# Optimization experiments

Measured on AMD Instinct MI355X. Metric: run time of the kernel, lower is better.

## Reference

```python
import jax, jax.numpy as jnp
import numpy as np
from jax import lax

B, T, D = 1, 2048, 2048
H, KVH, HD = 16, 4, 128
BETA = 0.9
ROPE_BASE = 10000.0


def _causal_prefix_ema(x, beta):
    # x: (B, T, D); m_t = beta * m_{t-1} + (1 - beta) * x_t, m_{-1} = 0
    def step(m, xt):
        m = beta * m + (1.0 - beta) * xt
        return m, m
    _, ys = lax.scan(step, jnp.zeros_like(x[:, 0]), jnp.swapaxes(x, 0, 1))
    return jnp.swapaxes(ys, 0, 1)


def _rotate_half(x):
    x1, x2 = jnp.split(x, 2, axis=-1)
    return jnp.concatenate([-x2, x1], axis=-1)


def _rope_cos_sin(t, hd, dtype):
    inv_freq = 1.0 / (ROPE_BASE ** (jnp.arange(0, hd, 2, dtype=jnp.float32) / hd))
    freqs = jnp.arange(t, dtype=jnp.float32)[:, None] * inv_freq[None, :]  # (T, HD/2)
    emb = jnp.concatenate([freqs, freqs], axis=-1)  # (T, HD)
    return jnp.cos(emb).astype(dtype)[None, None], jnp.sin(emb).astype(dtype)[None, None]


def setup_inputs() -> dict:
    key = jax.random.key(0)
    ks = jax.random.split(key, 8)
    std = 0.02
    return {
        "hidden_states": jax.random.normal(ks[0], (B, T, D), jnp.float32),
        "Wq": jax.random.normal(ks[1], (D, H * HD), jnp.float32) * std,
        "Wk": jax.random.normal(ks[2], (D, KVH * HD), jnp.float32) * std,
        "Wv": jax.random.normal(ks[3], (D, KVH * HD), jnp.float32) * std,
        "Wo": jax.random.normal(ks[4], (H * HD, D), jnp.float32) * std,
        "Wr1": jax.random.normal(ks[5], (D, D // 2), jnp.float32) * std,
        "br1": jnp.zeros((D // 2,), jnp.float32),
        "Wr2": jax.random.normal(ks[6], (D // 2, 2), jnp.float32) * std,
        "br2": jnp.zeros((2,), jnp.float32),
    }


def reference(hidden_states, Wq, Wk, Wv, Wo, Wr1, br1, Wr2, br2):
    b, t, d = hidden_states.shape
    q = hidden_states @ Wq  # (B, T, H*HD)

    # multi-level memories: l1 = raw, l2 = causal prefix EMA
    l2 = _causal_prefix_ema(hidden_states, BETA)

    # router MLP on q + softmax over levels
    h = jax.nn.silu(q @ Wr1 + br1)
    lam = jax.nn.softmax(h @ Wr2 + br2, axis=-1)  # (B, T, 2)
    fused = lam[..., 0:1] * hidden_states + lam[..., 1:2] * l2

    # shape to heads
    q_s = q.reshape(b, t, H, HD).transpose(0, 2, 1, 3)                 # (B, H, T, HD)
    k_s = (fused @ Wk).reshape(b, t, KVH, HD).transpose(0, 2, 1, 3)    # (B, KVH, T, HD)
    v_s = (fused @ Wv).reshape(b, t, KVH, HD).transpose(0, 2, 1, 3)

    # RoPE
    cos, sin = _rope_cos_sin(t, HD, q_s.dtype)
    q_s = q_s * cos + _rotate_half(q_s) * sin
    k_s = k_s * cos + _rotate_half(k_s) * sin

    # repeat kv for GQA
    n_rep = H // KVH
    k_s = jnp.repeat(k_s, n_rep, axis=1)
    v_s = jnp.repeat(v_s, n_rep, axis=1)

    # causal SDPA
    scale = 1.0 / jnp.sqrt(jnp.asarray(HD, q_s.dtype))
    scores = jnp.einsum("bhqd,bhkd->bhqk", q_s, k_s) * scale
    causal = jnp.tril(jnp.ones((t, t), dtype=bool))
    scores = jnp.where(causal[None, None], scores, jnp.finfo(scores.dtype).min)
    attn = jax.nn.softmax(scores, axis=-1)
    out = jnp.einsum("bhqk,bhkd->bhqd", attn, v_s)  # (B, H, T, HD)

    out = out.transpose(0, 2, 1, 3).reshape(b, t, H * HD)
    return out @ Wo
```

## Files before the change

### kernel.cpp

```cpp
#include <hip/hip_runtime.h>
#include <hip/hip_bf16.h>

#define T_SEQ 2048
#define D_MODEL 2048
#define NH 16
#define NKVH 4
#define HD 128

typedef __attribute__((ext_vector_type(8))) short bf16x8;
typedef __attribute__((ext_vector_type(4))) float f32x4;

static __device__ __forceinline__ short f32_to_bf16(float f) {
    unsigned u = __float_as_uint(f);
    u += 0x7fffu + ((u >> 16) & 1u);
    return (short)(u >> 16);
}
static __device__ __forceinline__ float bf16_to_f32(short s) {
    return __uint_as_float(((unsigned)(unsigned short)s) << 16);
}
static __device__ __forceinline__ void gl_to_lds16(const void* g, void* l) {
    __builtin_amdgcn_global_load_lds(
        (const __attribute__((address_space(1))) unsigned int*)g,
        (__attribute__((address_space(3))) unsigned int*)l, 16, 0, 0);
}

template<int BN>
__global__ __launch_bounds__(256, 2) void gemm_bt_kernel(
    const short* __restrict__ A, const short* __restrict__ Bt,
    float* __restrict__ Cf, short* __restrict__ Cb,
    int M, int N, int K, const float* __restrict__ bias, int act)
{
    constexpr int NI = BN / 64;
    constexpr int BCH = BN / 32;
    __shared__ short Alds[3][64 * 64];
    __shared__ short Blds[3][BN * 64];

    const int tid = threadIdx.x;
    const int wave = tid >> 6, lane = tid & 63;
    const int l16 = lane & 15, quad = lane >> 4;
    const int wn = wave * (BN / 4);
    const int m0 = blockIdx.y * 64, n0 = blockIdx.x * BN;
    const int niter = K >> 6;

    f32x4 acc[4][NI] = {};

    #pragma unroll
    for (int st = 0; st < 2; ++st) {
        int kk0 = st << 6;
        #pragma unroll
        for (int p = 0; p < 2; ++p) {
            int li = p * 256 + tid;
            int row = li >> 3, sc = li & 7;
            gl_to_lds16(A + (size_t)(m0 + row) * K + kk0 + ((sc ^ (row & 7)) * 8),
                        &Alds[st][(size_t)(p * 256 + wave * 64) * 8]);
        }
        #pragma unroll
        for (int p = 0; p < BCH; ++p) {
            int li = p * 256 + tid;
            int row = li >> 3, sc = li & 7;
            gl_to_lds16(Bt + (size_t)(n0 + row) * K + kk0 + ((sc ^ (row & 7)) * 8),
                        &Blds[st][(size_t)(p * 256 + wave * 64) * 8]);
        }
    }

    int cur = 0, stg = 2;
    for (int t = 0; t < niter; ++t) {
        if (t + 1 < niter) {
            if constexpr (BN == 128)
                asm volatile("s_waitcnt vmcnt(6)\n\ts_barrier" ::: "memory");
            else
                asm volatile("s_waitcnt vmcnt(4)\n\ts_barrier" ::: "memory");
        } else {
            asm volatile("s_waitcnt vmcnt(0)\n\ts_barrier" ::: "memory");
        }

        if (t + 2 < niter) {
            int k1 = (t + 2) << 6;
            #pragma unroll
            for (int p = 0; p < 2; ++p) {
                int li = p * 256 + tid;
                int row = li >> 3, sc = li & 7;
                gl_to_lds16(A + (size_t)(m0 + row) * K + k1 + ((sc ^ (row & 7)) * 8),
                            &Alds[stg][(size_t)(p * 256 + wave * 64) * 8]);
            }
            #pragma unroll
            for (int p = 0; p < BCH; ++p) {
                int li = p * 256 + tid;
                int row = li >> 3, sc = li & 7;
                gl_to_lds16(Bt + (size_t)(n0 + row) * K + k1 + ((sc ^ (row & 7)) * 8),
                            &Blds[stg][(size_t)(p * 256 + wave * 64) * 8]);
            }
        }

        const short* Ab = Alds[cur];
        const short* Bb = Blds[cur];
        #pragma unroll
        for (int kk = 0; kk < 2; ++kk) {
            bf16x8 a[4], b[NI];
            #pragma unroll
            for (int i = 0; i < 4; ++i)
                a[i] = *(const bf16x8*)
                    &Ab[(size_t)(i * 16 + l16) * 64 + (((kk * 4 + quad) ^ (l16 & 7)) * 8)];
            #pragma unroll
            for (int i = 0; i < NI; ++i)
                b[i] = *(const bf16x8*)
                    &Bb[(size_t)(wn + i * 16 + l16) * 64 + (((kk * 4 + quad) ^ (l16 & 7)) * 8)];
            #pragma unroll
            for (int mi = 0; mi < 4; ++mi)
                #pragma unroll
                for (int ni = 0; ni < NI; ++ni)
                    acc[mi][ni] = __builtin_amdgcn_mfma_f32_16x16x32_bf16(
                        a[mi], b[ni], acc[mi][ni], 0, 0, 0);
        }
        cur = (cur == 2) ? 0 : cur + 1;
        stg = (stg == 2) ? 0 : stg + 1;
    }

    #pragma unroll
    for (int mi = 0; mi < 4; ++mi) {
        #pragma unroll
        for (int ni = 0; ni < NI; ++ni) {
            int col = n0 + wn + ni * 16 + l16;
            float bv = bias ? bias[col] : 0.0f;
            #pragma unroll
            for (int r = 0; r < 4; ++r) {
                int row = m0 + mi * 16 + quad * 4 + r;
                float x = acc[mi][ni][r] + bv;
                if (act) x = x / (1.0f + __expf(-x));
                size_t o = (size_t)row * N + col;
                if (Cf) Cf[o] = x;
                if (Cb) Cb[o] = f32_to_bf16(x);
            }
        }
    }
}

__global__ __launch_bounds__(256) void transpose_all_kernel(
    const float* __restrict__ Wq, const float* __restrict__ Wk,
    const float* __restrict__ Wv, const float* __restrict__ Wr1,
    const float* __restrict__ Wo, short* __restrict__ Wq_t,
    short* __restrict__ Wkv_t, short* __restrict__ Wr1_t,
    short* __restrict__ Wo_t)
{
    __shared__ float tile[32][33];
    int bx = blockIdx.x;
    const float* src; short* dst; int ld, cb;
    if (bx < 64)       { src = Wq;  dst = Wq_t;  ld = 2048; cb = bx; }
    else if (bx < 80)  { src = Wk;  dst = Wkv_t; ld = 512;  cb = bx - 64; }
    else if (bx < 96)  { src = Wv;  dst = Wkv_t + (size_t)512 * 2048; ld = 512; cb = bx - 80; }
    else if (bx < 128) { src = Wr1; dst = Wr1_t; ld = 1024; cb = bx - 96; }
    else               { src = Wo;  dst = Wo_t;  ld = 2048; cb = bx - 128; }
    int c0 = cb * 32, r0 = blockIdx.y * 32;
    int t = threadIdx.x;
    int r = t >> 3, c4 = (t & 7) * 4;
    float4 v = *(const float4*)&src[(size_t)(r0 + r) * ld + c0 + c4];
    tile[r][c4 + 0] = v.x; tile[r][c4 + 1] = v.y;
    tile[r][c4 + 2] = v.z; tile[r][c4 + 3] = v.w;
    __syncthreads();
    short o[4];
    #pragma unroll
    for (int j = 0; j < 4; ++j) o[j] = f32_to_bf16(tile[c4 + j][r]);
    *(uint2*)&dst[(size_t)(c0 + r) * 2048 + r0 + c4] = *(const uint2*)o;
}

__global__ __launch_bounds__(256) void transpose_bf_kernel(
    const short* __restrict__ src, int ld, short* __restrict__ dst, int ldd)
{
    __shared__ float tile[32][33];
    int r0 = blockIdx.y * 32, c0 = blockIdx.x * 32;
    int x = threadIdx.x & 31, y = threadIdx.x >> 5;
    #pragma unroll
    for (int i = 0; i < 4; ++i)
        tile[y + i * 8][x] = bf16_to_f32(src[(size_t)(r0 + y + i * 8) * ld + c0 + x]);
    __syncthreads();
    #pragma unroll
    for (int i = 0; i < 4; ++i)
        dst[(size_t)(c0 + y + i * 8) * ldd + r0 + x] = f32_to_bf16(tile[x][y + i * 8]);
}

__global__ __launch_bounds__(256) void ema_kernel(const float* __restrict__ hs,
                                                  float* __restrict__ l2,
                                                  short* __restrict__ hs_b)
{
    int d = blockIdx.y * 256 + threadIdx.x;
    int t0 = blockIdx.x * 128;
    int ts = t0 - 192; if (ts < 0) ts = 0;
    float m = 0.0f;
    for (int tb = ts; tb < t0; tb += 16) {
        float buf[16];
        #pragma unroll
        for (int j = 0; j < 16; ++j) buf[j] = hs[(size_t)(tb + j) * D_MODEL + d];
        #pragma unroll
        for (int j = 0; j < 16; ++j) m = 0.9f * m + 0.1f * buf[j];
    }
    for (int tb = t0; tb < t0 + 128; tb += 16) {
        float buf[16];
        #pragma unroll
        for (int j = 0; j < 16; ++j) buf[j] = hs[(size_t)(tb + j) * D_MODEL + d];
        #pragma unroll
        for (int j = 0; j < 16; ++j) hs_b[(size_t)(tb + j) * D_MODEL + d] = f32_to_bf16(buf[j]);
        #pragma unroll
        for (int j = 0; j < 16; ++j) { m = 0.9f * m + 0.1f * buf[j]; buf[j] = m; }
        #pragma unroll
        for (int j = 0; j < 16; ++j) l2[(size_t)(tb + j) * D_MODEL + d] = buf[j];
    }
}

__global__ __launch_bounds__(64) void lam_kernel(
    const short* __restrict__ h, const float* __restrict__ Wr2,
    const float* __restrict__ br2, float* __restrict__ lam)
{
    int t = blockIdx.x;
    int lane = threadIdx.x;
    float z0 = 0.0f, z1 = 0.0f;
    for (int i = lane; i < 1024; i += 64) {
        float hv = bf16_to_f32(h[(size_t)t * 1024 + i]);
        z0 += hv * Wr2[i * 2 + 0];
        z1 += hv * Wr2[i * 2 + 1];
    }
    #pragma unroll
    for (int off = 1; off < 64; off <<= 1) {
        z0 += __shfl_xor(z0, off);
        z1 += __shfl_xor(z1, off);
    }
    if (lane == 0) {
        z0 += br2[0]; z1 += br2[1];
        float mx = fmaxf(z0, z1);
        float e0 = expf(z0 - mx), e1 = expf(z1 - mx);
        float inv = 1.0f / (e0 + e1);
        lam[t * 2 + 0] = e0 * inv;
        lam[t * 2 + 1] = e1 * inv;
    }
}

__global__ void fuse_kernel(const float* __restrict__ hs, const float* __restrict__ l2,
                            const float* __restrict__ lam, short* __restrict__ fused)
{
    int idx = blockIdx.x * blockDim.x + threadIdx.x;
    int t = idx >> 9;
    float a0 = lam[t * 2 + 0], a1 = lam[t * 2 + 1];
    float4 a = ((const float4*)hs)[idx];
    float4 b = ((const float4*)l2)[idx];
    short o[4] = {f32_to_bf16(a0 * a.x + a1 * b.x), f32_to_bf16(a0 * a.y + a1 * b.y),
                  f32_to_bf16(a0 * a.z + a1 * b.z), f32_to_bf16(a0 * a.w + a1 * b.w)};
    *(uint2*)(fused + (size_t)idx * 4) = *(const uint2*)o;
}

__global__ void rope_q_kernel(const short* __restrict__ q, short* __restrict__ qr)
{
    int idx = blockIdx.x * blockDim.x + threadIdx.x;
    int d = idx & 63;
    int h = (idx >> 6) & 15;
    int t = idx >> 10;
    float fr = (float)t * __expf(-(float)d * 0.14391156831212787f);
    float s, c;
    sincosf(fr, &s, &c);
    const float sc = 0.08838834764831845f;
    const short* src = q + (size_t)t * D_MODEL + h * HD;
    float x1 = bf16_to_f32(src[d]) * sc, x2 = bf16_to_f32(src[d + 64]) * sc;
    short* dst = qr + ((size_t)h * T_SEQ + t) * HD;
    dst[d]      = f32_to_bf16(x1 * c - x2 * s);
    dst[d + 64] = f32_to_bf16(x2 * c + x1 * s);
}

__global__ void rope_k_kernel(const short* __restrict__ kv, short* __restrict__ kr)
{
    int idx = blockIdx.x * blockDim.x + threadIdx.x;
    int d = idx & 63;
    int kh = (idx >> 6) & 3;
    int t = idx >> 8;
    float fr = (float)t * __expf(-(float)d * 0.14391156831212787f);
    float s, c;
    sincosf(fr, &s, &c);
    const short* src = kv + (size_t)t * 1024 + kh * HD;
    float x1 = bf16_to_f32(src[d]), x2 = bf16_to_f32(src[d + 64]);
    short* dst = kr + ((size_t)kh * T_SEQ + t) * HD;
    dst[d]      = f32_to_bf16(x1 * c - x2 * s);
    dst[d + 64] = f32_to_bf16(x2 * c + x1 * s);
}

__global__ __launch_bounds__(512, 2) void attn_kernel(
    const short* __restrict__ Qr, const short* __restrict__ Kr,
    const short* __restrict__ Vt, short* __restrict__ Out)
{
    const int h = blockIdx.x;
    const int y = blockIdx.y;
    const int kvh = h >> 2;
    const int tid = threadIdx.x;
    const int wave = tid >> 6, lane = tid & 63;
    const int l16 = lane & 15, quad = lane >> 4;
    const int wq = wave & 1;
    const int wk = wave >> 1;

    __shared__ __align__(16) char smem[147456];
    short* Klds = (short*)smem;
    short* Vlds = (short*)(smem + 65536);
    short* Plds = (short*)(smem + 131072);

    const short* kbase = Kr + (size_t)kvh * T_SEQ * HD;
    const short* vbase = Vt + (size_t)kvh * HD * T_SEQ;

    #pragma unroll 1
    for (int ph = 0; ph < 2; ++ph) {
        const int qt32 = ph ? (31 - y) : y;
        const int qbase = qt32 * 64 + wq * 32;
        const int n = (qt32 >> 1) + 1;
        const int ko = wk * 32;

        bf16x8 qf[2][4];
        #pragma unroll
        for (int m = 0; m < 2; ++m) {
            const short* qrow = Qr + ((size_t)h * T_SEQ + qbase + m * 16 + l16) * HD;
            #pragma unroll
            for (int kc = 0; kc < 4; ++kc)
                qf[m][kc] = *(const bf16x8*)&qrow[kc * 32 + quad * 8];
        }
        f32x4 o[2][8] = {};
        float lsum[2][4] = {};

        __syncthreads();

        {
            #pragma unroll
            for (int p = 0; p < 4; ++p) {
                int li = p * 512 + tid;
                int row = li >> 4, gs = (li & 15) ^ (row & 15);
                gl_to_lds16(kbase + (size_t)row * HD + gs * 8,
                            &Klds[(size_t)(p * 512 + wave * 64) * 8]);
            }
            #pragma unroll
            for (int p = 0; p < 4; ++p) {
                int li = p * 512 + tid;
                int row = li >> 4, gs = (li & 15) ^ (row & 15);
                gl_to_lds16(vbase + (size_t)row * T_SEQ + gs * 8,
                            &Vlds[(size_t)(p * 512 + wave * 64) * 8]);
            }
        }

        for (int t = 0; t < n; ++t) {
            asm volatile("s_waitcnt vmcnt(0)\n\ts_barrier" ::: "memory");

            if (t + 1 < n) {
                int kv1 = (t + 1) << 7;
                int nb = (t + 1) & 1;
                const short* ks = kbase + (size_t)kv1 * HD;
                #pragma unroll
                for (int p = 0; p < 4; ++p) {
                    int li = p * 512 + tid;
                    int row = li >> 4, gs = (li & 15) ^ (row & 15);
                    gl_to_lds16(ks + (size_t)row * HD + gs * 8,
                                &Klds[(size_t)(nb * 16384 + (p * 512 + wave * 64) * 8)]);
                }
                #pragma unroll
                for (int p = 0; p < 4; ++p) {
                    int li = p * 512 + tid;
                    int row = li >> 4, gs = (li & 15) ^ (row & 15);
                    gl_to_lds16(vbase + (size_t)row * T_SEQ + kv1 + gs * 8,
                                &Vlds[(size_t)(nb * 16384 + (p * 512 + wave * 64) * 8)]);
                }
            }

            const short* Kb = Klds + (size_t)(t & 1) * 16384;
            const short* Vb = Vlds + (size_t)(t & 1) * 16384;

            f32x4 s[2][2];
            #pragma unroll
            for (int m = 0; m < 2; ++m)
                #pragma unroll
                for (int ni = 0; ni < 2; ++ni) s[m][ni] = (f32x4){0, 0, 0, 0};
            __builtin_amdgcn_s_setprio(1);
            #pragma unroll
            for (int ni = 0; ni < 2; ++ni)
                #pragma unroll
                for (int kc = 0; kc < 4; ++kc) {
                    bf16x8 b = *(const bf16x8*)
                        &Kb[(size_t)(ko + ni * 16 + l16) * 128 + (((kc * 4 + quad) ^ l16) * 8)];
                    s[0][ni] = __builtin_amdgcn_mfma_f32_16x16x32_bf16(qf[0][kc], b, s[0][ni], 0, 0, 0);
                    s[1][ni] = __builtin_amdgcn_mfma_f32_16x16x32_bf16(qf[1][kc], b, s[1][ni], 0, 0, 0);
                }
            __builtin_amdgcn_s_setprio(0);

            if (t == n - 1) {
                int kvg0 = (t << 7) + ko;
                #pragma unroll
                for (int m = 0; m < 2; ++m)
                    #pragma unroll
                    for (int ni = 0; ni < 2; ++ni) {
                        int kvg = kvg0 + ni * 16 + l16;
                        #pragma unroll
                        for (int r = 0; r < 4; ++r) {
                            int qg = qbase + m * 16 + quad * 4 + r;
                            float p = (kvg <= qg) ? __expf(s[m][ni][r]) : 0.0f;
                            lsum[m][r] += p;
                            int prow = quad * 4 + r, pcol = ni * 16 + l16;
                            int slot = (pcol >> 3) ^ (prow & 3) ^ quad;
                            Plds[wave * 1024 + (m * 16 + prow) * 32 +
                                 slot * 8 + (pcol & 7)] = f32_to_bf16(p);
                        }
                    }
            } else {
                #pragma unroll
                for (int m = 0; m < 2; ++m)
                    #pragma unroll
                    for (int ni = 0; ni < 2; ++ni)
                        #pragma unroll
                        for (int r = 0; r < 4; ++r) {
                            float p = __expf(s[m][ni][r]);
                            lsum[m][r] += p;
                            int prow = quad * 4 + r, pcol = ni * 16 + l16;
                            int slot = (pcol >> 3) ^ (prow & 3) ^ quad;
                            Plds[wave * 1024 + (m * 16 + prow) * 32 +
                                 slot * 8 + (pcol & 7)] = f32_to_bf16(p);
                        }
            }
            asm volatile("s_waitcnt lgkmcnt(0)" ::: "memory");

            __builtin_amdgcn_s_setprio(1);
            {
                int slot0 = quad ^ (l16 & 3) ^ ((l16 >> 2) & 3);
                bf16x8 pa0 = *(const bf16x8*)
                    &Plds[wave * 1024 + l16 * 32 + slot0 * 8];
                bf16x8 pa1 = *(const bf16x8*)
                    &Plds[wave * 1024 + (16 + l16) * 32 + slot0 * 8];
                #pragma unroll
                for (int d8 = 0; d8 < 8; ++d8) {
                    bf16x8 b = *(const bf16x8*)
                        &Vb[(size_t)(d8 * 16 + l16) * 128 +
                            (((wk * 4 + quad) ^ l16) * 8)];
                    o[0][d8] = __builtin_amdgcn_mfma_f32_16x16x32_bf16(pa0, b, o[0][d8], 0, 0, 0);
                    o[1][d8] = __builtin_amdgcn_mfma_f32_16x16x32_bf16(pa1, b, o[1][d8], 0, 0, 0);
                }
            }
            __builtin_amdgcn_s_setprio(0);
        }

        __syncthreads();
        float* Ox = (float*)smem;
        float* Lx = (float*)(smem + 101376);
        if (wk) {
            int base = (wq * 3 + wk - 1) * 32;
            #pragma unroll
            for (int m = 0; m < 2; ++m)
                #pragma unroll
                for (int d8 = 0; d8 < 8; ++d8)
                    #pragma unroll
                    for (int r = 0; r < 4; ++r)
                        Ox[(base + m * 16 + quad * 4 + r) * 132 + d8 * 16 + l16] = o[m][d8][r];
            #pragma unroll
            for (int m = 0; m < 2; ++m)
                #pragma unroll
                for (int r = 0; r < 4; ++r)
                    Lx[(base + m * 16 + quad * 4 + r) * 16 + l16] = lsum[m][r];
        }
        __syncthreads();
        if (wk == 0) {
            #pragma unroll
            for (int j = 0; j < 3; ++j)
                #pragma unroll
                for (int m = 0; m < 2; ++m)
                    #pragma unroll
                    for (int d8 = 0; d8 < 8; ++d8)
                        #pragma unroll
                        for (int r = 0; r < 4; ++r)
                            o[m][d8][r] += Ox[((wq * 3 + j) * 32 + m * 16 + quad * 4 + r) * 132
                                              + d8 * 16 + l16];
            #pragma unroll
            for (int m = 0; m < 2; ++m)
                #pragma unroll
                for (int r = 0; r < 4; ++r) {
                    #pragma unroll
                    for (int j = 0; j < 3; ++j)
                        lsum[m][r] += Lx[((wq * 3 + j) * 32 + m * 16 + quad * 4 + r) * 16 + l16];
                    #pragma unroll
                    for (int off = 1; off < 16; off <<= 1)
                        lsum[m][r] += __shfl_xor(lsum[m][r], off);
                    lsum[m][r] = 1.0f / lsum[m][r];
                }
            #pragma unroll
            for (int m = 0; m < 2; ++m)
                #pragma unroll
                for (int d8 = 0; d8 < 8; ++d8)
                    #pragma unroll
                    for (int r = 0; r < 4; ++r) {
                        int row = qbase + m * 16 + quad * 4 + r;
                        Out[(size_t)row * D_MODEL + h * HD + d8 * 16 + l16] =
                            f32_to_bf16(o[m][d8][r] * lsum[m][r]);
                    }
        }
    }
}

extern "C" void kernel_launch(void* const* d_in, const int* in_sizes, int n_in,
                              void* d_out, int out_size, void* d_ws, size_t ws_size,
                              hipStream_t stream)
{
    const float* hs  = (const float*)d_in[0];
    const float* Wq  = (const float*)d_in[1];
    const float* Wk  = (const float*)d_in[2];
    const float* Wv  = (const float*)d_in[3];
    const float* Wo  = (const float*)d_in[4];
    const float* Wr1 = (const float*)d_in[5];
    const float* br1 = (const float*)d_in[6];
    const float* Wr2 = (const float*)d_in[7];
    const float* br2 = (const float*)d_in[8];
    float* out = (float*)d_out;

    char* w = (char*)d_ws;
    const size_t MB = 1u << 20;
    float* l2_f     = (float*)(w + 0 * MB);
    short* hs_bf    = (short*)(w + 16 * MB);
    short* Wq_t     = (short*)(w + 24 * MB);
    short* Wkv_t    = (short*)(w + 32 * MB);
    short* Wr1_t    = (short*)(w + 36 * MB);
    short* Wo_t     = (short*)(w + 40 * MB);
    short* q_bf     = (short*)(w + 48 * MB);
    short* h_bf     = (short*)(w + 56 * MB);
    short* fused_bf = (short*)(w + 60 * MB);
    short* kv_bf    = (short*)(w + 68 * MB);
    short* qr       = (short*)(w + 72 * MB);
    short* kr       = (short*)(w + 80 * MB);
    short* vr       = (short*)(w + 82 * MB);
    float* lam_f    = (float*)(w + 84 * MB);
    short* attn_bf  = hs_bf;

    transpose_all_kernel<<<dim3(192, 64), 256, 0, stream>>>(
        Wq, Wk, Wv, Wr1, Wo, Wq_t, Wkv_t, Wr1_t, Wo_t);

    ema_kernel<<<dim3(T_SEQ / 128, D_MODEL / 256), 256, 0, stream>>>(hs, l2_f, hs_bf);

    gemm_bt_kernel<128><<<dim3(16, 32), 256, 0, stream>>>(
        hs_bf, Wq_t, nullptr, q_bf, 2048, 2048, 2048, nullptr, 0);

    gemm_bt_kernel<64><<<dim3(16, 32), 256, 0, stream>>>(
        q_bf, Wr1_t, nullptr, h_bf, 2048, 1024, 2048, br1, 1);

    lam_kernel<<<T_SEQ, 64, 0, stream>>>(h_bf, Wr2, br2, lam_f);

    fuse_kernel<<<(T_SEQ * D_MODEL / 4) / 256, 256, 0, stream>>>(hs, l2_f, lam_f, fused_bf);

    gemm_bt_kernel<64><<<dim3(16, 32), 256, 0, stream>>>(
        fused_bf, Wkv_t, nullptr, kv_bf, 2048, 1024, 2048, nullptr, 0);

    rope_q_kernel<<<(T_SEQ * NH * 64) / 256, 256, 0, stream>>>(q_bf, qr);
    rope_k_kernel<<<(T_SEQ * NKVH * 64) / 256, 256, 0, stream>>>(kv_bf, kr);
    transpose_bf_kernel<<<dim3(16, 64), 256, 0, stream>>>(kv_bf + 512, 1024, vr, 2048);

    attn_kernel<<<dim3(NH, 16), 512, 0, stream>>>(qr, kr, vr, attn_bf);

    gemm_bt_kernel<128><<<dim3(16, 32), 256, 0, stream>>>(
        attn_bf, Wo_t, out, nullptr, 2048, 2048, 2048, nullptr, 0);
}
```

Before: 313.4 us.

## Fuse lambda into fuse kernel, merge RoPE/transpose kernels, unswizzle P LDS

Folds the router softmax (lam) computation into the fuse kernel, so each block recomputes the per-token lambda redundantly and the separate launch and lam buffer go away. Merges rope_q, rope_k and the V transpose into a single launch. Halves the EMA block size to give it more blocks. In attention, it hoists the V fragment loads ahead of the P writes and replaces the XOR-swizzled P layout with a padded stride-40 layout, which grows shared memory use and may change bank conflicts.

New measurement: 305.5 us. 2.5% less time.

```diff
diff --git a/kernel.cpp b/kernel.cpp
--- a/kernel.cpp
+++ b/kernel.cpp
@@ -163,26 +163,11 @@
     *(uint2*)&dst[(size_t)(c0 + r) * 2048 + r0 + c4] = *(const uint2*)o;
 }
 
-__global__ __launch_bounds__(256) void transpose_bf_kernel(
-    const short* __restrict__ src, int ld, short* __restrict__ dst, int ldd)
-{
-    __shared__ float tile[32][33];
-    int r0 = blockIdx.y * 32, c0 = blockIdx.x * 32;
-    int x = threadIdx.x & 31, y = threadIdx.x >> 5;
-    #pragma unroll
-    for (int i = 0; i < 4; ++i)
-        tile[y + i * 8][x] = bf16_to_f32(src[(size_t)(r0 + y + i * 8) * ld + c0 + x]);
-    __syncthreads();
-    #pragma unroll
-    for (int i = 0; i < 4; ++i)
-        dst[(size_t)(c0 + y + i * 8) * ldd + r0 + x] = f32_to_bf16(tile[x][y + i * 8]);
-}
-
-__global__ __launch_bounds__(256) void ema_kernel(const float* __restrict__ hs,
+__global__ __launch_bounds__(128) void ema_kernel(const float* __restrict__ hs,
                                                   float* __restrict__ l2,
                                                   short* __restrict__ hs_b)
 {
-    int d = blockIdx.y * 256 + threadIdx.x;
+    int d = blockIdx.y * 128 + threadIdx.x;
     int t0 = blockIdx.x * 128;
     int ts = t0 - 192; if (ts < 0) ts = 0;
     float m = 0.0f;
@@ -206,39 +191,44 @@
     }
 }
 
-__global__ __launch_bounds__(64) void lam_kernel(
+__global__ __launch_bounds__(256) void fuse_kernel(
+    const float* __restrict__ hs, const float* __restrict__ l2,
     const short* __restrict__ h, const float* __restrict__ Wr2,
-    const float* __restrict__ br2, float* __restrict__ lam)
-{
-    int t = blockIdx.x;
-    int lane = threadIdx.x;
+    const float* __restrict__ br2, short* __restrict__ fused)
+{
+    const int tid = threadIdx.x;
+    const int t = blockIdx.x >> 1;
+
     float z0 = 0.0f, z1 = 0.0f;
-    for (int i = lane; i < 1024; i += 64) {
-        float hv = bf16_to_f32(h[(size_t)t * 1024 + i]);
-        z0 += hv * Wr2[i * 2 + 0];
-        z1 += hv * Wr2[i * 2 + 1];
+    {
+        const short* hr = h + (size_t)t * 1024;
+        short4 hv4 = *(const short4*)&hr[tid * 4];
+        const float2* w2 = (const float2*)Wr2;
+        #pragma unroll
+        for (int j = 0; j < 4; ++j) {
+            float hv = bf16_to_f32(((const short*)&hv4)[j]);
+            float2 w = w2[tid * 4 + j];
+            z0 += hv * w.x;
+            z1 += hv * w.y;
+        }
     }
     #pragma unroll
     for (int off = 1; off < 64; off <<= 1) {
         z0 += __shfl_xor(z0, off);
         z1 += __shfl_xor(z1, off);
     }
-    if (lane == 0) {
-        z0 += br2[0]; z1 += br2[1];
-        float mx = fmaxf(z0, z1);
-        float e0 = expf(z0 - mx), e1 = expf(z1 - mx);
-        float inv = 1.0f / (e0 + e1);
-        lam[t * 2 + 0] = e0 * inv;
-        lam[t * 2 + 1] = e1 * inv;
-    }
-}
-
-__global__ void fuse_kernel(const float* __restrict__ hs, const float* __restrict__ l2,
-                            const float* __restrict__ lam, short* __restrict__ fused)
-{
-    int idx = blockIdx.x * blockDim.x + threadIdx.x;
-    int t = idx >> 9;
-    float a0 = lam[t * 2 + 0], a1 = lam[t * 2 + 1];
+    __shared__ float red[2][4];
+    int wave = tid >> 6, lane = tid & 63;
+    if (lane == 0) { red[0][wave] = z0; red[1][wave] = z1; }
+    __syncthreads();
+    z0 = red[0][0] + red[0][1] + red[0][2] + red[0][3] + br2[0];
+    z1 = red[1][0] + red[1][1] + red[1][2] + red[1][3] + br2[1];
+    float mx = fmaxf(z0, z1);
+    float e0 = expf(z0 - mx), e1 = expf(z1 - mx);
+    float inv = 1.0f / (e0 + e1);
+    float a0 = e0 * inv, a1 = e1 * inv;
+
+    int idx = blockIdx.x * 256 + tid;
     float4 a = ((const float4*)hs)[idx];
     float4 b = ((const float4*)l2)[idx];
     short o[4] = {f32_to_bf16(a0 * a.x + a1 * b.x), f32_to_bf16(a0 * a.y + a1 * b.y),
@@ -246,37 +236,52 @@
     *(uint2*)(fused + (size_t)idx * 4) = *(const uint2*)o;
 }
 
-__global__ void rope_q_kernel(const short* __restrict__ q, short* __restrict__ qr)
-{
-    int idx = blockIdx.x * blockDim.x + threadIdx.x;
-    int d = idx & 63;
-    int h = (idx >> 6) & 15;
-    int t = idx >> 10;
-    float fr = (float)t * __expf(-(float)d * 0.14391156831212787f);
-    float s, c;
-    sincosf(fr, &s, &c);
-    const float sc = 0.08838834764831845f;
-    const short* src = q + (size_t)t * D_MODEL + h * HD;
-    float x1 = bf16_to_f32(src[d]) * sc, x2 = bf16_to_f32(src[d + 64]) * sc;
-    short* dst = qr + ((size_t)h * T_SEQ + t) * HD;
-    dst[d]      = f32_to_bf16(x1 * c - x2 * s);
-    dst[d + 64] = f32_to_bf16(x2 * c + x1 * s);
-}
-
-__global__ void rope_k_kernel(const short* __restrict__ kv, short* __restrict__ kr)
-{
-    int idx = blockIdx.x * blockDim.x + threadIdx.x;
-    int d = idx & 63;
-    int kh = (idx >> 6) & 3;
-    int t = idx >> 8;
-    float fr = (float)t * __expf(-(float)d * 0.14391156831212787f);
-    float s, c;
-    sincosf(fr, &s, &c);
-    const short* src = kv + (size_t)t * 1024 + kh * HD;
-    float x1 = bf16_to_f32(src[d]), x2 = bf16_to_f32(src[d + 64]);
-    short* dst = kr + ((size_t)kh * T_SEQ + t) * HD;
-    dst[d]      = f32_to_bf16(x1 * c - x2 * s);
-    dst[d + 64] = f32_to_bf16(x2 * c + x1 * s);
+__global__ __launch_bounds__(256) void pp_kernel(
+    const short* __restrict__ q, const short* __restrict__ kv,
+    short* __restrict__ qr, short* __restrict__ kr, short* __restrict__ vr)
+{
+    int bx = blockIdx.x;
+    if (bx < 8192) {
+        int idx = bx * 256 + threadIdx.x;
+        int d = idx & 63;
+        int h = (idx >> 6) & 15;
+        int t = idx >> 10;
+        float fr = (float)t * __expf(-(float)d * 0.14391156831212787f);
+        float s, c;
+        sincosf(fr, &s, &c);
+        const float sc = 0.08838834764831845f;
+        const short* src = q + (size_t)t * D_MODEL + h * HD;
+        float x1 = bf16_to_f32(src[d]) * sc, x2 = bf16_to_f32(src[d + 64]) * sc;
+        short* dst = qr + ((size_t)h * T_SEQ + t) * HD;
+        dst[d]      = f32_to_bf16(x1 * c - x2 * s);
+        dst[d + 64] = f32_to_bf16(x2 * c + x1 * s);
+    } else if (bx < 10240) {
+        int idx = (bx - 8192) * 256 + threadIdx.x;
+        int d = idx & 63;
+        int kh = (idx >> 6) & 3;
+        int t = idx >> 8;
+        float fr = (float)t * __expf(-(float)d * 0.14391156831212787f);
+        float s, c;
+        sincosf(fr, &s, &c);
+        const short* src = kv + (size_t)t * 1024 + kh * HD;
+        float x1 = bf16_to_f32(src[d]), x2 = bf16_to_f32(src[d + 64]);
+        short* dst = kr + ((size_t)kh * T_SEQ + t) * HD;
+        dst[d]      = f32_to_bf16(x1 * c - x2 * s);
+        dst[d + 64] = f32_to_bf16(x2 * c + x1 * s);
+    } else {
+        __shared__ float tile[32][33];
+        int b2 = bx - 10240;
+        int c0 = (b2 & 15) * 32, r0 = (b2 >> 4) * 32;
+        const short* src = kv + 512;
+        int x = threadIdx.x & 31, y = threadIdx.x >> 5;
+        #pragma unroll
+        for (int i = 0; i < 4; ++i)
+            tile[y + i * 8][x] = bf16_to_f32(src[(size_t)(r0 + y + i * 8) * 1024 + c0 + x]);
+        __syncthreads();
+        #pragma unroll
+        for (int i = 0; i < 4; ++i)
+            vr[(size_t)(c0 + y + i * 8) * 2048 + r0 + x] = f32_to_bf16(tile[x][y + i * 8]);
+    }
 }
 
 __global__ __launch_bounds__(512, 2) void attn_kernel(
@@ -292,7 +297,7 @@
     const int wq = wave & 1;
     const int wk = wave >> 1;
 
-    __shared__ __align__(16) char smem[147456];
+    __shared__ __align__(16) char smem[151552];
     short* Klds = (short*)smem;
     short* Vlds = (short*)(smem + 65536);
     short* Plds = (short*)(smem + 131072);
@@ -380,6 +385,13 @@
                 }
             __builtin_amdgcn_s_setprio(0);
 
+            bf16x8 vb[8];
+            #pragma unroll
+            for (int d8 = 0; d8 < 8; ++d8)
+                vb[d8] = *(const bf16x8*)
+                    &Vb[(size_t)(d8 * 16 + l16) * 128 + (((wk * 4 + quad) ^ l16) * 8)];
+
+            short* Pw = Plds + wave * 1280;
             if (t == n - 1) {
                 int kvg0 = (t << 7) + ko;
                 #pragma unroll
@@ -392,10 +404,8 @@
                             int qg = qbase + m * 16 + quad * 4 + r;
                             float p = (kvg <= qg) ? __expf(s[m][ni][r]) : 0.0f;
                             lsum[m][r] += p;
-                            int prow = quad * 4 + r, pcol = ni * 16 + l16;
-                            int slot = (pcol >> 3) ^ (prow & 3) ^ quad;
-                            Plds[wave * 1024 + (m * 16 + prow) * 32 +
-                                 slot * 8 + (pcol & 7)] = f32_to_bf16(p);
+                            Pw[(m * 16 + quad * 4 + r) * 40 + ni * 16 + l16] =
+                                f32_to_bf16(p);
                         }
                     }
             } else {
@@ -407,28 +417,22 @@
                         for (int r = 0; r < 4; ++r) {
                             float p = __expf(s[m][ni][r]);
                             lsum[m][r] += p;
-                            int prow = quad * 4 + r, pcol = ni * 16 + l16;
-                            int slot = (pcol >> 3) ^ (prow & 3) ^ quad;
-                            Plds[wave * 1024 + (m * 16 + prow) * 32 +
-                                 slot * 8 + (pcol & 7)] = f32_to_bf16(p);
+                            Pw[(m * 16 + quad * 4 + r) * 40 + ni * 16 + l16] =
+                                f32_to_bf16(p);
                         }
             }
             asm volatile("s_waitcnt lgkmcnt(0)" ::: "memory");
 
             __builtin_amdgcn_s_setprio(1);
             {
-                int slot0 = quad ^ (l16 & 3) ^ ((l16 >> 2) & 3);
-                bf16x8 pa0 = *(const bf16x8*)
-                    &Plds[wave * 1024 + l16 * 32 + slot0 * 8];
-                bf16x8 pa1 = *(const bf16x8*)
-                    &Plds[wave * 1024 + (16 + l16) * 32 + slot0 * 8];
+                bf16x8 pa0 = *(const bf16x8*)&Pw[l16 * 40 + quad * 8];
+                bf16x8 pa1 = *(const bf16x8*)&Pw[(16 + l16) * 40 + quad * 8];
                 #pragma unroll
                 for (int d8 = 0; d8 < 8; ++d8) {
-                    bf16x8 b = *(const bf16x8*)
-                        &Vb[(size_t)(d8 * 16 + l16) * 128 +
-                            (((wk * 4 + quad) ^ l16) * 8)];
-                    o[0][d8] = __builtin_amdgcn_mfma_f32_16x16x32_bf16(pa0, b, o[0][d8], 0, 0, 0);
-                    o[1][d8] = __builtin_amdgcn_mfma_f32_16x16x32_bf16(pa1, b, o[1][d8], 0, 0, 0);
+                    o[0][d8] = __builtin_amdgcn_mfma_f32_16x16x32_bf16(
+                        pa0, vb[d8], o[0][d8], 0, 0, 0);
+                    o[1][d8] = __builtin_amdgcn_mfma_f32_16x16x32_bf16(
+                        pa1, vb[d8], o[1][d8], 0, 0, 0);
                 }
             }
             __builtin_amdgcn_s_setprio(0);
@@ -520,13 +524,12 @@
     short* qr       = (short*)(w + 72 * MB);
     short* kr       = (short*)(w + 80 * MB);
     short* vr       = (short*)(w + 82 * MB);
-    float* lam_f    = (float*)(w + 84 * MB);
     short* attn_bf  = hs_bf;
 
     transpose_all_kernel<<<dim3(192, 64), 256, 0, stream>>>(
         Wq, Wk, Wv, Wr1, Wo, Wq_t, Wkv_t, Wr1_t, Wo_t);
 
-    ema_kernel<<<dim3(T_SEQ / 128, D_MODEL / 256), 256, 0, stream>>>(hs, l2_f, hs_bf);
+    ema_kernel<<<dim3(T_SEQ / 128, D_MODEL / 128), 128, 0, stream>>>(hs, l2_f, hs_bf);
 
     gemm_bt_kernel<128><<<dim3(16, 32), 256, 0, stream>>>(
         hs_bf, Wq_t, nullptr, q_bf, 2048, 2048, 2048, nullptr, 0);
@@ -534,16 +537,13 @@
     gemm_bt_kernel<64><<<dim3(16, 32), 256, 0, stream>>>(
         q_bf, Wr1_t, nullptr, h_bf, 2048, 1024, 2048, br1, 1);
 
-    lam_kernel<<<T_SEQ, 64, 0, stream>>>(h_bf, Wr2, br2, lam_f);
-
-    fuse_kernel<<<(T_SEQ * D_MODEL / 4) / 256, 256, 0, stream>>>(hs, l2_f, lam_f, fused_bf);
+    fuse_kernel<<<(T_SEQ * D_MODEL / 4) / 256, 256, 0, stream>>>(
+        hs, l2_f, h_bf, Wr2, br2, fused_bf);
 
     gemm_bt_kernel<64><<<dim3(16, 32), 256, 0, stream>>>(
         fused_bf, Wkv_t, nullptr, kv_bf, 2048, 1024, 2048, nullptr, 0);
 
-    rope_q_kernel<<<(T_SEQ * NH * 64) / 256, 256, 0, stream>>>(q_bf, qr);
-    rope_k_kernel<<<(T_SEQ * NKVH * 64) / 256, 256, 0, stream>>>(kv_bf, kr);
-    transpose_bf_kernel<<<dim3(16, 64), 256, 0, stream>>>(kv_bf + 512, 1024, vr, 2048);
+    pp_kernel<<<11264, 256, 0, stream>>>(q_bf, kv_bf, qr, kr, vr);
 
     attn_kernel<<<dim3(NH, 16), 512, 0, stream>>>(qr, kr, vr, attn_bf);
 
```
